# Kernel tuning notes

Measured on AMD Instinct MI355X. Metric: run time of the kernel, lower is better.

Reference implementation:

```python
import jax, jax.numpy as jnp
import numpy as np

T = 2048           # tokens (single prefill sequence)
HIDDEN = 2048
H = 16             # num heads
D_NOPE = 128
D_ROPE = 64
D_V = 128
KV_LORA = 512
EPS = 1e-6
ROPE_THETA = 10000.0


def setup_inputs() -> dict:
    key = jax.random.key(0)
    ks = jax.random.split(key, 7)
    s = 0.02
    return {
        "positions": jnp.arange(T, dtype=jnp.int64) if jax.config.jax_enable_x64 else jnp.arange(T, dtype=jnp.int32),
        "hidden_states": jax.random.normal(ks[0], (T, HIDDEN), dtype=jnp.float32),
        "w_q": jax.random.normal(ks[1], (HIDDEN, H * (D_NOPE + D_ROPE)), dtype=jnp.float32) * s,
        "w_kv_a": jax.random.normal(ks[2], (HIDDEN, KV_LORA + D_ROPE), dtype=jnp.float32) * s,
        "kv_a_ln_w": jax.random.uniform(ks[3], (KV_LORA,), dtype=jnp.float32, minval=0.5, maxval=1.5),
        "w_kv_b": jax.random.normal(ks[4], (KV_LORA, H * (D_NOPE + D_V)), dtype=jnp.float32) * s,
        "w_o": jax.random.normal(ks[5], (H * D_V, HIDDEN), dtype=jnp.float32) * s,
    }


def _rms_norm(x, w):
    var = jnp.mean(jnp.square(x), axis=-1, keepdims=True)
    return x * jax.lax.rsqrt(var + EPS) * w


def _rope_nonneox(x, positions):
    # x: [..., D_ROPE], GPT-J (interleaved) style rotation
    inv_freq = 1.0 / (ROPE_THETA ** (jnp.arange(0, D_ROPE, 2, dtype=jnp.float32) / D_ROPE))
    freqs = positions.astype(jnp.float32)[:, None] * inv_freq  # [T, D_ROPE//2]
    cos, sin = jnp.cos(freqs), jnp.sin(freqs)
    # broadcast over head dim if present
    while cos.ndim < x.ndim:
        cos, sin = cos[:, None], sin[:, None]
    x1, x2 = x[..., 0::2], x[..., 1::2]
    o1 = x1 * cos - x2 * sin
    o2 = x2 * cos + x1 * sin
    return jnp.stack([o1, o2], axis=-1).reshape(x.shape)


def reference(positions, hidden_states, w_q, w_kv_a, kv_a_ln_w, w_kv_b, w_o):
    scaling = (D_NOPE + D_ROPE) ** -0.5
    # q projection (q_lora_rank is None branch)
    q = (hidden_states @ w_q).reshape(T, H, D_NOPE + D_ROPE)
    q_nope, q_pe = q[..., :D_NOPE], q[..., D_NOPE:]
    # compressed KV latent
    latent = hidden_states @ w_kv_a                 # [T, KV_LORA + D_ROPE]
    kv_a = _rms_norm(latent[:, :KV_LORA], kv_a_ln_w)
    k_pe = latent[:, KV_LORA:]                      # [T, D_ROPE], shared across heads
    # decompress to per-head k_nope and v (kv_b_proj)
    kv = (kv_a @ w_kv_b).reshape(T, H, D_NOPE + D_V)
    k_nope, v = kv[..., :D_NOPE], kv[..., D_NOPE:]
    # non-neox RoPE
    q_pe = _rope_nonneox(q_pe, positions)
    k_pe = _rope_nonneox(k_pe, positions)           # [T, D_ROPE]
    # concat rope parts (k_pe broadcast over heads)
    q_full = jnp.concatenate([q_nope, q_pe], axis=-1)                         # [T,H,192]
    k_full = jnp.concatenate([k_nope, jnp.broadcast_to(k_pe[:, None, :], (T, H, D_ROPE))], axis=-1)
    # causal MHA
    scores = jnp.einsum("qhd,khd->hqk", q_full, k_full) * scaling
    causal = positions[:, None] >= positions[None, :]
    scores = jnp.where(causal[None], scores, -jnp.inf)
    attn = jax.nn.softmax(scores, axis=-1)
    out = jnp.einsum("hqk,khd->qhd", attn, v).reshape(T, H * D_V)
    return out @ w_o
```

## Files before the change

### kernel.cpp

```cpp
#include <hip/hip_runtime.h>
#include <hip/hip_bf16.h>
#include <stdint.h>

#define T_SEQ   2048
#define NHEAD   16
#define NPAD1   3712

typedef short bf16x8  __attribute__((ext_vector_type(8)));
typedef float f32x4   __attribute__((ext_vector_type(4)));
typedef float f32x16  __attribute__((ext_vector_type(16)));

__device__ __forceinline__ unsigned short f2bf(float f) {
  union { float f; uint32_t u; } v; v.f = f;
  uint32_t u = v.u;
  uint32_t r = u + 0x7FFF + ((u >> 16) & 1);
  return (unsigned short)(r >> 16);
}

__device__ __forceinline__ void async16(const void* g, void* l) {
  __builtin_amdgcn_global_load_lds(
      (const __attribute__((address_space(1))) void*)g,
      (__attribute__((address_space(3))) void*)l, 16, 0, 0);
}

__device__ __forceinline__ void tr32(const float* __restrict__ in,
    unsigned short* __restrict__ out, int R, int C, int bx, int by,
    float (*tile)[33], int tid) {
  int r0 = bx * 32, c0 = by * 32;
  int tx = tid & 31, ty = tid >> 5;
  for (int i = 0; i < 4; i++)
    tile[ty + i * 8][tx] = in[(size_t)(r0 + ty + i * 8) * C + c0 + tx];
  __syncthreads();
  for (int i = 0; i < 4; i++) {
    int c = ty + i * 8;
    out[(size_t)(c0 + c) * R + r0 + tx] = f2bf(tile[tx][c]);
  }
}

__global__ __launch_bounds__(256) void prep_kernel(
    const float* __restrict__ hs, const float* __restrict__ w_q,
    const float* __restrict__ w_kv_a, const float* __restrict__ w_kv_b,
    const float* __restrict__ w_o, const int* __restrict__ positions,
    unsigned short* __restrict__ hs_bf, unsigned short* __restrict__ wcat_t,
    unsigned short* __restrict__ wkvb_t, unsigned short* __restrict__ wo_t,
    float* __restrict__ rope_tab) {
  __shared__ float tile[32][33];
  int bid = blockIdx.x, tid = threadIdx.x;
  if (bid < 4096) {
    int i = (bid * 256 + tid) * 4;
    float4 v = *(const float4*)(hs + i);
    ushort4 o; o.x = f2bf(v.x); o.y = f2bf(v.y); o.z = f2bf(v.z); o.w = f2bf(v.w);
    *(ushort4*)(hs_bf + i) = o;
  } else if (bid < 4096 + 6144) {
    int l = bid - 4096;
    tr32(w_q, wcat_t, 2048, 3072, l & 63, l >> 6, tile, tid);
  } else if (bid < 4096 + 6144 + 1152) {
    int l = bid - (4096 + 6144);
    tr32(w_kv_a, wcat_t + (size_t)3072 * 2048, 2048, 576, l & 63, l >> 6, tile, tid);
  } else if (bid < 4096 + 6144 + 1152 + 2048) {
    int l = bid - (4096 + 6144 + 1152);
    tr32(w_kv_b, wkvb_t, 512, 4096, l & 15, l >> 4, tile, tid);
  } else if (bid < 4096 + 6144 + 1152 + 2048 + 4096) {
    int l = bid - (4096 + 6144 + 1152 + 2048);
    tr32(w_o, wo_t, 2048, 2048, l & 63, l >> 6, tile, tid);
  } else if (bid < 17600) {
    int l = bid - (4096 + 6144 + 1152 + 2048 + 4096);
    uint4 z = (uint4){0, 0, 0, 0};
    *(uint4*)(wcat_t + (size_t)3648 * 2048 + (size_t)(l * 256 + tid) * 8) = z;
  } else {
    int l = bid - 17600;
    int t = l * 8 + (tid >> 5), p = tid & 31;
    float pos = (float)positions[t];
    float inv_freq = powf(10000.f, -(float)(2 * p) / 64.f);
    float c, s; sincosf(pos * inv_freq, &s, &c);
    rope_tab[(size_t)t * 64 + 2 * p]     = c;
    rope_tab[(size_t)t * 64 + 2 * p + 1] = s;
  }
}

template<int TM, int EPI>
__global__ __launch_bounds__(256) void gemm_bt_kernel(
    const unsigned short* __restrict__ A, const unsigned short* __restrict__ B,
    void* __restrict__ Cv, int M, int N, int K,
    unsigned short* __restrict__ q_full, const float* __restrict__ rope_tab) {
  constexpr int MT = TM / 32;
  __shared__ __align__(16) unsigned short Asm[2][TM * 32];
  __shared__ __align__(16) unsigned short Bsm[2][128 * 32];
  int tid = threadIdx.x, wid = tid >> 6, lane = tid & 63;
  int lrow = lane & 15, lquad = lane >> 4;
  int m0 = blockIdx.x * TM, n0 = blockIdx.y * 128;
  int wm = (wid & 1) * (TM / 2), wn = (wid >> 1) * 64;

  int row_s = tid >> 2, cc_s = tid & 3;
  const unsigned short* Ag0 = A + (size_t)(m0 + row_s) * K + cc_s * 8;
  const unsigned short* Ag1 = A + (size_t)(m0 + row_s + 64) * K + cc_s * 8;
  const unsigned short* Bg0 = B + (size_t)(n0 + row_s) * K + cc_s * 8;
  const unsigned short* Bg1 = B + (size_t)(n0 + row_s + 64) * K + cc_s * 8;

  f32x4 acc[MT][4];
  #pragma unroll
  for (int i = 0; i < MT; i++)
    #pragma unroll
    for (int j = 0; j < 4; j++) acc[i][j] = (f32x4){0.f,0.f,0.f,0.f};

  async16(Ag0, &Asm[0][tid * 8]);
  if (TM == 128) async16(Ag1, &Asm[0][2048 + tid * 8]);
  async16(Bg0, &Bsm[0][tid * 8]);
  async16(Bg1, &Bsm[0][2048 + tid * 8]);

  int cur = 0;
  for (int k0 = 0; k0 < K; k0 += 32) {
    __syncthreads();
    if (k0 + 32 < K) {
      int nxt = cur ^ 1, kk = k0 + 32;
      async16(Ag0 + kk, &Asm[nxt][tid * 8]);
      if (TM == 128) async16(Ag1 + kk, &Asm[nxt][2048 + tid * 8]);
      async16(Bg0 + kk, &Bsm[nxt][tid * 8]);
      async16(Bg1 + kk, &Bsm[nxt][2048 + tid * 8]);
    }
    const unsigned short* As = Asm[cur];
    const unsigned short* Bs = Bsm[cur];
    bf16x8 af[MT], bfr[4];
    #pragma unroll
    for (int mt = 0; mt < MT; mt++)
      af[mt] = *(const bf16x8*)(As + (wm + mt * 16 + lrow) * 32 + lquad * 8);
    #pragma unroll
    for (int nt = 0; nt < 4; nt++)
      bfr[nt] = *(const bf16x8*)(Bs + (wn + nt * 16 + lrow) * 32 + lquad * 8);
    #pragma unroll
    for (int mt = 0; mt < MT; mt++)
      #pragma unroll
      for (int nt = 0; nt < 4; nt++)
        acc[mt][nt] = __builtin_amdgcn_mfma_f32_16x16x32_bf16(af[mt], bfr[nt], acc[mt][nt], 0, 0, 0);
    cur ^= 1;
  }

  if constexpr (EPI == 2) {
    const float scaling = 0.07216878364870323f;
    float* qlat = (float*)Cv;
    #pragma unroll
    for (int nt = 0; nt < 4; nt++) {
      int colb = n0 + wn + nt * 16;
      if (colb >= 3072) {
        int col = colb - 3072 + lrow;
        #pragma unroll
        for (int mt = 0; mt < MT; mt++) {
          int row = m0 + wm + mt * 16 + lquad * 4;
          #pragma unroll
          for (int r = 0; r < 4; r++)
            qlat[(size_t)(row + r) * 640 + col] = acc[mt][nt][r];
        }
      } else {
        int h = colb / 192;
        int hm = colb - h * 192;
        unsigned short* qh = q_full + (size_t)h * T_SEQ * 192;
        if (hm < 128) {
          #pragma unroll
          for (int mt = 0; mt < MT; mt++) {
            int row = m0 + wm + mt * 16 + lquad * 4;
            #pragma unroll
            for (int r = 0; r < 4; r++)
              qh[(size_t)(row + r) * 192 + hm + lrow] = f2bf(acc[mt][nt][r] * scaling);
          }
        } else {
          int p2 = (hm - 128 + lrow) & ~1;
          int odd = lrow & 1;
          #pragma unroll
          for (int mt = 0; mt < MT; mt++) {
            int row = m0 + wm + mt * 16 + lquad * 4;
            #pragma unroll
            for (int r = 0; r < 4; r++) {
              int rg = row + r;
              float c = rope_tab[(size_t)rg * 64 + p2];
              float s = rope_tab[(size_t)rg * 64 + p2 + 1];
              float own = acc[mt][nt][r];
              float oth = __shfl_xor(own, 1, 64);
              float o = odd ? (own * c + oth * s)
                            : (own * c - oth * s);
              qh[(size_t)rg * 192 + hm + lrow] = f2bf(o * scaling);
            }
          }
        }
      }
    }
  } else {
    #pragma unroll
    for (int mt = 0; mt < MT; mt++)
      #pragma unroll
      for (int nt = 0; nt < 4; nt++) {
        int row = m0 + wm + mt * 16 + lquad * 4;
        int col = n0 + wn + nt * 16 + lrow;
        #pragma unroll
        for (int r = 0; r < 4; r++) {
          if (EPI == 1)
            ((unsigned short*)Cv)[(size_t)(row + r) * N + col] = f2bf(acc[mt][nt][r]);
          else
            ((float*)Cv)[(size_t)(row + r) * N + col] = acc[mt][nt][r];
        }
      }
  }
}

__global__ __launch_bounds__(256) void postproc1_kernel(
    const float* __restrict__ q_lat,
    const float* __restrict__ ln_w,
    const float* __restrict__ rope_tab,
    unsigned short* __restrict__ kv_a,
    unsigned short* __restrict__ k_pe)
{
  int t = blockIdx.x, tid = threadIdx.x;
  const float* row = q_lat + (size_t)t * 640;

  float v0 = row[tid], v1 = row[256 + tid];
  float ss = v0 * v0 + v1 * v1;
  for (int m = 1; m < 64; m <<= 1) ss += __shfl_xor(ss, m, 64);
  __shared__ float red[4];
  if ((tid & 63) == 0) red[tid >> 6] = ss;
  __shared__ float kro[64];
  if (tid < 32) {
    float c = rope_tab[(size_t)t * 64 + 2 * tid];
    float s = rope_tab[(size_t)t * 64 + 2 * tid + 1];
    float x1 = row[512 + 2 * tid], x2 = row[512 + 2 * tid + 1];
    kro[2 * tid]     = x1 * c - x2 * s;
    kro[2 * tid + 1] = x2 * c + x1 * s;
  }
  __syncthreads();
  float rstd = rsqrtf((red[0] + red[1] + red[2] + red[3]) * (1.f / 512.f) + 1e-6f);
  kv_a[(size_t)t * 512 + tid]       = f2bf(v0 * rstd * ln_w[tid]);
  kv_a[(size_t)t * 512 + 256 + tid] = f2bf(v1 * rstd * ln_w[256 + tid]);
  if (tid < 64) k_pe[(size_t)t * 64 + tid] = f2bf(kro[tid]);
}

__global__ __launch_bounds__(256) void kvpost_kernel(
    const unsigned short* __restrict__ kv_b,
    const unsigned short* __restrict__ k_pe,
    unsigned short* __restrict__ k_full,
    unsigned short* __restrict__ v_t) {
  __shared__ unsigned short tile[32][41];
  int bid = blockIdx.x, tid = threadIdx.x;
  if (bid < 3072) {
    int idx = bid * 256 + tid;
    int cc = idx % 24, rest = idx / 24;
    int t = rest & (T_SEQ - 1), h = rest >> 11;
    uint4 v = (cc < 16)
        ? *(const uint4*)(kv_b + (size_t)t * 4096 + h * 256 + cc * 8)
        : *(const uint4*)(k_pe + (size_t)t * 64 + (cc - 16) * 8);
    *(uint4*)(k_full + (size_t)idx * 8) = v;
  } else {
    int l = bid - 3072;
    int h = l >> 8, t0 = (l & 63) * 32, d0 = ((l >> 6) & 3) * 32;
    int tx = tid & 31, ty = tid >> 5;
    for (int i = 0; i < 4; i++)
      tile[ty + i * 8][tx] = kv_b[(size_t)(t0 + ty + i * 8) * 4096 + h * 256 + 128 + d0 + tx];
    __syncthreads();
    for (int i = 0; i < 4; i++)
      v_t[((size_t)h * 128 + d0 + ty + i * 8) * T_SEQ + t0 + tx] = tile[tx][ty + i * 8];
  }
}

#define PP 76
__global__ __launch_bounds__(256, 2) void flash_kernel(
    const unsigned short* __restrict__ q_full,
    const unsigned short* __restrict__ k_full,
    const unsigned short* __restrict__ v_t,
    unsigned short* __restrict__ attn_out)
{
  __shared__ __align__(16) unsigned short Ksm[2][1536 * 8];
  __shared__ __align__(16) unsigned short Vsm[1024 * 8];
  __shared__ __align__(16) unsigned short Psm[64 * PP];
  __shared__ float Lred[2][64];
  int h = blockIdx.x;
  int y = blockIdx.y;
  int qb = (y < 16) ? (31 - y) : (y - 16);
  int tid = threadIdx.x, wid = tid >> 6, lane = tid & 63;
  int l31 = lane & 31, l5 = lane >> 5, x7 = l31 & 7;
  int rq = wid & 1, kq = wid >> 1;

  const unsigned short* kh = k_full + (size_t)h * T_SEQ * 192;
  const unsigned short* vh = v_t    + (size_t)h * 128 * T_SEQ;

  int gK[6], gV[4];
  #pragma unroll
  for (int j = 0; j < 6; j++) {
    int s = tid + j * 256, row = s / 24, cm = s - row * 24;
    gK[j] = row * 192 + (cm ^ (row & 7)) * 8;
  }
  #pragma unroll
  for (int j = 0; j < 4; j++) {
    int s = tid + j * 256, d = s >> 3;
    gV[j] = d * T_SEQ + ((s & 7) ^ (d & 7)) * 8;
  }
  int kxo[12];
  #pragma unroll
  for (int kc = 0; kc < 12; kc++)
    kxo[kc] = (kq * 32 + l31) * 192 + ((kc * 2 + l5) ^ x7) * 8;
  int vxb[2];
  #pragma unroll
  for (int ntv = 0; ntv < 2; ntv++) vxb[ntv] = (kq * 64 + ntv * 32 + l31) * 64;

  bf16x8 qf[12];
  {
    const unsigned short* qrow =
        q_full + ((size_t)h * T_SEQ + qb * 64 + rq * 32 + l31) * 192 + l5 * 8;
    #pragma unroll
    for (int kc = 0; kc < 12; kc++) qf[kc] = *(const bf16x8*)(qrow + kc * 16);
  }
  f32x16 oacc[2];
  for (int i = 0; i < 2; i++) oacc[i] = (f32x16)(0.f);
  float lsum[16];
  #pragma unroll
  for (int r = 0; r < 16; r++) lsum[r] = 0.f;
  int rl[16];
  #pragma unroll
  for (int r = 0; r < 16; r++) rl[r] = (r & 3) + 8 * (r >> 2) + 4 * l5;

  #pragma unroll
  for (int j = 0; j < 6; j++) async16(kh + gK[j], &Ksm[0][(tid + j * 256) * 8]);

  int cur = 0;
  for (int kb = 0; kb <= qb; kb++) {
    __syncthreads();
    {
      const unsigned short* vb = vh + kb * 64;
      #pragma unroll
      for (int j = 0; j < 4; j++) async16(vb + gV[j], &Vsm[(tid + j * 256) * 8]);
    }
    const unsigned short* Ks = Ksm[cur];
    f32x16 sacc = (f32x16)(0.f);
    #pragma unroll
    for (int kc = 0; kc < 12; kc++) {
      bf16x8 kf = *(const bf16x8*)(Ks + kxo[kc]);
      sacc = __builtin_amdgcn_mfma_f32_32x32x16_bf16(qf[kc], kf, sacc, 0, 0, 0);
    }
    if (kb == qb) {
      int col_g = kb * 64 + kq * 32 + l31;
      int row_b = qb * 64 + rq * 32;
      #pragma unroll
      for (int r = 0; r < 16; r++)
        if (col_g > row_b + rl[r]) sacc[r] = -1e30f;
    }
    #pragma unroll
    for (int r = 0; r < 16; r++) {
      float p = __expf(sacc[r]);
      sacc[r] = p;
      lsum[r] += p;
    }
    #pragma unroll
    for (int r = 0; r < 16; r++)
      Psm[(rq * 32 + rl[r]) * PP + kq * 32 + l31] = f2bf(sacc[r]);
    __syncthreads();
    if (kb < qb) {
      const unsigned short* kb1 = kh + (size_t)(kb + 1) * 64 * 192;
      #pragma unroll
      for (int j = 0; j < 6; j++) async16(kb1 + gK[j], &Ksm[cur ^ 1][(tid + j * 256) * 8]);
    }
    #pragma unroll
    for (int kc = 0; kc < 4; kc++) {
      bf16x8 pf = *(const bf16x8*)(Psm + (rq * 32 + l31) * PP + kc * 16 + l5 * 8);
      #pragma unroll
      for (int ntv = 0; ntv < 2; ntv++) {
        bf16x8 vf = *(const bf16x8*)(Vsm + vxb[ntv] + ((kc * 2 + l5) ^ x7) * 8);
        oacc[ntv] = __builtin_amdgcn_mfma_f32_32x32x16_bf16(pf, vf, oacc[ntv], 0, 0, 0);
      }
    }
    cur ^= 1;
  }

  #pragma unroll
  for (int r = 0; r < 16; r++) {
    float s = lsum[r];
    s += __shfl_xor(s, 1, 64);
    s += __shfl_xor(s, 2, 64);
    s += __shfl_xor(s, 4, 64);
    s += __shfl_xor(s, 8, 64);
    s += __shfl_xor(s, 16, 64);
    lsum[r] = s;
  }
  if (l31 == 0)
    #pragma unroll
    for (int r = 0; r < 16; r++) Lred[kq][rq * 32 + rl[r]] = lsum[r];
  __syncthreads();
  #pragma unroll
  for (int r = 0; r < 16; r++) {
    int row_l = rq * 32 + rl[r];
    float inv = 1.f / (Lred[0][row_l] + Lred[1][row_l]);
    int row_g = qb * 64 + row_l;
    #pragma unroll
    for (int ntv = 0; ntv < 2; ntv++)
      attn_out[(size_t)row_g * 2048 + h * 128 + kq * 64 + ntv * 32 + l31] =
          f2bf(oacc[ntv][r] * inv);
  }
}

extern "C" void kernel_launch(void* const* d_in, const int* in_sizes, int n_in,
                              void* d_out, int out_size, void* d_ws, size_t ws_size,
                              hipStream_t stream) {
  const int*   positions = (const int*)d_in[0];
  const float* hs     = (const float*)d_in[1];
  const float* w_q    = (const float*)d_in[2];
  const float* w_kv_a = (const float*)d_in[3];
  const float* ln_w   = (const float*)d_in[4];
  const float* w_kv_b = (const float*)d_in[5];
  const float* w_o    = (const float*)d_in[6];
  float* out = (float*)d_out;

  char* ws = (char*)d_ws;
  size_t off = 0;
  auto alloc = [&](size_t bytes) { void* p = ws + off; off += (bytes + 255) & ~(size_t)255; return p; };
  unsigned short* hs_bf   = (unsigned short*)alloc((size_t)2048 * 2048 * 2);
  unsigned short* wcat_t  = (unsigned short*)alloc((size_t)NPAD1 * 2048 * 2);
  float*          q_lat   = (float*)alloc((size_t)2048 * 640 * 4);
  unsigned short* kv_a_bf = (unsigned short*)alloc((size_t)2048 * 512 * 2);
  unsigned short* wkvb_t  = (unsigned short*)alloc((size_t)4096 * 512 * 2);
  unsigned short* kv_b    = (unsigned short*)alloc((size_t)2048 * 4096 * 2);
  unsigned short* q_full  = (unsigned short*)alloc((size_t)NHEAD * 2048 * 192 * 2);
  unsigned short* k_pe    = (unsigned short*)alloc((size_t)2048 * 64 * 2);
  unsigned short* k_full  = (unsigned short*)alloc((size_t)NHEAD * 2048 * 192 * 2);
  unsigned short* v_t     = (unsigned short*)alloc((size_t)NHEAD * 128 * 2048 * 2);
  unsigned short* attn_o  = (unsigned short*)alloc((size_t)2048 * 2048 * 2);
  unsigned short* wo_t    = (unsigned short*)alloc((size_t)2048 * 2048 * 2);
  float*          rope_tab= (float*)alloc((size_t)2048 * 64 * 4);

  prep_kernel<<<17856, 256, 0, stream>>>(hs, w_q, w_kv_a, w_kv_b, w_o, positions,
                                         hs_bf, wcat_t, wkvb_t, wo_t, rope_tab);
  gemm_bt_kernel<128, 2><<<dim3(16, 29), 256, 0, stream>>>(
      hs_bf, wcat_t, q_lat, 2048, NPAD1, 2048, q_full, rope_tab);
  postproc1_kernel<<<2048, 256, 0, stream>>>(q_lat, ln_w, rope_tab, kv_a_bf, k_pe);
  gemm_bt_kernel<128, 1><<<dim3(16, 32), 256, 0, stream>>>(
      kv_a_bf, wkvb_t, kv_b, 2048, 4096, 512, nullptr, nullptr);
  kvpost_kernel<<<7168, 256, 0, stream>>>(kv_b, k_pe, k_full, v_t);
  flash_kernel<<<dim3(16, 32), 256, 0, stream>>>(q_full, k_full, v_t, attn_o);
  gemm_bt_kernel<64, 0><<<dim3(32, 16), 256, 0, stream>>>(
      attn_o, wo_t, out, 2048, 2048, 2048, nullptr, nullptr);
}
```

Baseline: 277.5 us.

## Load K directly from kv_b and k_pe in flash kernel; shrink GEMM M tiles

Drops the k_full materialization (a 12 MB copy that concatenated k_nope with a broadcast k_pe per head). The flash kernel now async-loads K tiles directly from kv_b and k_pe using per-slot pointers and strides. The Q/latent and kv_b GEMMs also switch from 128-row to 64-row tiles, doubling the grid for better CU occupancy. The strided reads from kv_b are less contiguous than the old packed layout, and smaller tiles give up some data reuse.

```diff
diff --git a/kernel.cpp b/kernel.cpp
--- a/kernel.cpp
+++ b/kernel.cpp
@@ -233,35 +233,23 @@
 
 __global__ __launch_bounds__(256) void kvpost_kernel(
     const unsigned short* __restrict__ kv_b,
-    const unsigned short* __restrict__ k_pe,
-    unsigned short* __restrict__ k_full,
     unsigned short* __restrict__ v_t) {
   __shared__ unsigned short tile[32][41];
-  int bid = blockIdx.x, tid = threadIdx.x;
-  if (bid < 3072) {
-    int idx = bid * 256 + tid;
-    int cc = idx % 24, rest = idx / 24;
-    int t = rest & (T_SEQ - 1), h = rest >> 11;
-    uint4 v = (cc < 16)
-        ? *(const uint4*)(kv_b + (size_t)t * 4096 + h * 256 + cc * 8)
-        : *(const uint4*)(k_pe + (size_t)t * 64 + (cc - 16) * 8);
-    *(uint4*)(k_full + (size_t)idx * 8) = v;
-  } else {
-    int l = bid - 3072;
-    int h = l >> 8, t0 = (l & 63) * 32, d0 = ((l >> 6) & 3) * 32;
-    int tx = tid & 31, ty = tid >> 5;
-    for (int i = 0; i < 4; i++)
-      tile[ty + i * 8][tx] = kv_b[(size_t)(t0 + ty + i * 8) * 4096 + h * 256 + 128 + d0 + tx];
-    __syncthreads();
-    for (int i = 0; i < 4; i++)
-      v_t[((size_t)h * 128 + d0 + ty + i * 8) * T_SEQ + t0 + tx] = tile[tx][ty + i * 8];
-  }
+  int l = blockIdx.x, tid = threadIdx.x;
+  int h = l >> 8, t0 = (l & 63) * 32, d0 = ((l >> 6) & 3) * 32;
+  int tx = tid & 31, ty = tid >> 5;
+  for (int i = 0; i < 4; i++)
+    tile[ty + i * 8][tx] = kv_b[(size_t)(t0 + ty + i * 8) * 4096 + h * 256 + 128 + d0 + tx];
+  __syncthreads();
+  for (int i = 0; i < 4; i++)
+    v_t[((size_t)h * 128 + d0 + ty + i * 8) * T_SEQ + t0 + tx] = tile[tx][ty + i * 8];
 }
 
 #define PP 76
 __global__ __launch_bounds__(256, 2) void flash_kernel(
     const unsigned short* __restrict__ q_full,
-    const unsigned short* __restrict__ k_full,
+    const unsigned short* __restrict__ kv_b,
+    const unsigned short* __restrict__ k_pe,
     const unsigned short* __restrict__ v_t,
     unsigned short* __restrict__ attn_out)
 {
@@ -276,15 +264,17 @@
   int l31 = lane & 31, l5 = lane >> 5, x7 = l31 & 7;
   int rq = wid & 1, kq = wid >> 1;
 
-  const unsigned short* kh = k_full + (size_t)h * T_SEQ * 192;
-  const unsigned short* vh = v_t    + (size_t)h * 128 * T_SEQ;
-
-  int gK[6], gV[4];
+  const unsigned short* vh = v_t + (size_t)h * 128 * T_SEQ;
+
+  const unsigned short* pK[6]; int sK[6];
   #pragma unroll
   for (int j = 0; j < 6; j++) {
     int s = tid + j * 256, row = s / 24, cm = s - row * 24;
-    gK[j] = row * 192 + (cm ^ (row & 7)) * 8;
-  }
+    int c = cm ^ (row & 7);
+    if (c < 16) { pK[j] = kv_b + (size_t)row * 4096 + h * 256 + c * 8; sK[j] = 64 * 4096; }
+    else        { pK[j] = k_pe + (size_t)row * 64 + (c - 16) * 8;      sK[j] = 64 * 64; }
+  }
+  int gV[4];
   #pragma unroll
   for (int j = 0; j < 4; j++) {
     int s = tid + j * 256, d = s >> 3;
@@ -315,7 +305,7 @@
   for (int r = 0; r < 16; r++) rl[r] = (r & 3) + 8 * (r >> 2) + 4 * l5;
 
   #pragma unroll
-  for (int j = 0; j < 6; j++) async16(kh + gK[j], &Ksm[0][(tid + j * 256) * 8]);
+  for (int j = 0; j < 6; j++) async16(pK[j], &Ksm[0][(tid + j * 256) * 8]);
 
   int cur = 0;
   for (int kb = 0; kb <= qb; kb++) {
@@ -350,9 +340,9 @@
       Psm[(rq * 32 + rl[r]) * PP + kq * 32 + l31] = f2bf(sacc[r]);
     __syncthreads();
     if (kb < qb) {
-      const unsigned short* kb1 = kh + (size_t)(kb + 1) * 64 * 192;
-      #pragma unroll
-      for (int j = 0; j < 6; j++) async16(kb1 + gK[j], &Ksm[cur ^ 1][(tid + j * 256) * 8]);
+      #pragma unroll
+      for (int j = 0; j < 6; j++)
+        async16(pK[j] + (size_t)(kb + 1) * sK[j], &Ksm[cur ^ 1][(tid + j * 256) * 8]);
     }
     #pragma unroll
     for (int kc = 0; kc < 4; kc++) {
@@ -415,7 +405,6 @@
   unsigned short* kv_b    = (unsigned short*)alloc((size_t)2048 * 4096 * 2);
   unsigned short* q_full  = (unsigned short*)alloc((size_t)NHEAD * 2048 * 192 * 2);
   unsigned short* k_pe    = (unsigned short*)alloc((size_t)2048 * 64 * 2);
-  unsigned short* k_full  = (unsigned short*)alloc((size_t)NHEAD * 2048 * 192 * 2);
   unsigned short* v_t     = (unsigned short*)alloc((size_t)NHEAD * 128 * 2048 * 2);
   unsigned short* attn_o  = (unsigned short*)alloc((size_t)2048 * 2048 * 2);
   unsigned short* wo_t    = (unsigned short*)alloc((size_t)2048 * 2048 * 2);
@@ -423,13 +412,13 @@
 
   prep_kernel<<<17856, 256, 0, stream>>>(hs, w_q, w_kv_a, w_kv_b, w_o, positions,
                                          hs_bf, wcat_t, wkvb_t, wo_t, rope_tab);
-  gemm_bt_kernel<128, 2><<<dim3(16, 29), 256, 0, stream>>>(
+  gemm_bt_kernel<64, 2><<<dim3(32, 29), 256, 0, stream>>>(
       hs_bf, wcat_t, q_lat, 2048, NPAD1, 2048, q_full, rope_tab);
   postproc1_kernel<<<2048, 256, 0, stream>>>(q_lat, ln_w, rope_tab, kv_a_bf, k_pe);
-  gemm_bt_kernel<128, 1><<<dim3(16, 32), 256, 0, stream>>>(
+  gemm_bt_kernel<64, 1><<<dim3(32, 32), 256, 0, stream>>>(
       kv_a_bf, wkvb_t, kv_b, 2048, 4096, 512, nullptr, nullptr);
-  kvpost_kernel<<<7168, 256, 0, stream>>>(kv_b, k_pe, k_full, v_t);
-  flash_kernel<<<dim3(16, 32), 256, 0, stream>>>(q_full, k_full, v_t, attn_o);
+  kvpost_kernel<<<4096, 256, 0, stream>>>(kv_b, v_t);
+  flash_kernel<<<dim3(16, 32), 256, 0, stream>>>(q_full, kv_b, k_pe, v_t, attn_o);
   gemm_bt_kernel<64, 0><<<dim3(32, 16), 256, 0, stream>>>(
       attn_o, wo_t, out, 2048, 2048, 2048, nullptr, nullptr);
 }
```

After: 276.8 us. No clear change (-0.3%).
